# Kernel optimization log

Hardware: AMD Instinct MI355X
Metric: run time of the kernel (lower is better)

## Reference

```python
import jax, jax.numpy as jnp
import numpy as np


def _quantum_act(x, act_w):
    # LearnedQuantumActivation, eval mode (no phase noise): softmax-weighted mix of 9 activations
    w = jax.nn.softmax(act_w)
    mish = x * jnp.tanh(jax.nn.softplus(x))
    return (w[0] * jax.nn.sigmoid(x) + w[1] * jax.nn.elu(x) + w[2] * jnp.tanh(x)
            + w[3] * jax.nn.relu(x) + w[4] * jax.nn.silu(x)
            + w[5] * jax.nn.gelu(x, approximate=False) + w[6] * jax.nn.selu(x)
            + w[7] * mish + w[8] * x)


def setup_inputs() -> dict:
    B, D, U, N = 1024, 1024, 2048, 4      # batch, input_dim, max_units, num_branches
    M, MD, O, H = 2048, 1024, 512, 64     # memory_size, memory_dim, output_dim, critic hidden
    key = jax.random.key(0)
    ks = jax.random.split(key, 16)
    g = lambda k, shape, s=0.02: jax.random.normal(k, shape, dtype=jnp.float32) * s
    return {
        "x": jax.random.normal(ks[0], (B, D), dtype=jnp.float32),
        "w": g(ks[1], (D, U, N)),
        "b": jnp.zeros((U, N), jnp.float32),
        "gate_w": g(ks[2], (D, N)), "gate_b": jnp.zeros((N,), jnp.float32),
        "act_w": jnp.ones((9,), jnp.float32),
        "mask": jnp.ones((U,), jnp.float32),          # neuron_mask, initial_units == max_units
        "mem": g(ks[3], (M, MD), 0.05),
        "att_w": g(ks[4], (U, M)), "att_b": jnp.zeros((M,), jnp.float32),
        "write_w": g(ks[5], (U, MD)), "write_b": jnp.zeros((MD,), jnp.float32),
        "update_gate": jnp.full((M,), 0.5, jnp.float32),
        "out_w": g(ks[6], (U, O)), "out_b": jnp.zeros((O,), jnp.float32),
        "cw1": g(ks[7], (MD, H // 2)), "cb1": jnp.zeros((H // 2,), jnp.float32),
        "cw2": g(ks[8], (O, H // 2)), "cb2": jnp.zeros((H // 2,), jnp.float32),
        "cw3": g(ks[9], (U, H // 2)), "cb3": jnp.zeros((H // 2,), jnp.float32),
        "cw4": g(ks[10], (3 * (H // 2), H)), "cb4": jnp.zeros((H,), jnp.float32),
        "cw5": g(ks[11], (H, 2)), "cb5": jnp.zeros((2,), jnp.float32),
        "meta_threshold": jnp.float32(0.5),
    }


def reference(x, w, b, gate_w, gate_b, act_w, mask, mem, att_w, att_b,
              write_w, write_b, update_gate, out_w, out_b,
              cw1, cb1, cw2, cb2, cw3, cb3, cw4, cb4, cw5, cb5, meta_threshold):
    # Dendritic plastic dense: per-branch projections mixed by a learned softmax branch gate
    pre = jnp.einsum('bi,iun->bun', x, w) + b               # (B, U, N)
    gate = jax.nn.softmax(x @ gate_w + gate_b, axis=-1)     # (B, N)
    hidden = _quantum_act(jnp.einsum('bun,bn->bu', pre, gate), act_w) * mask  # (B, U)
    # Episodic memory read + write (write is returned instead of in-place assign)
    read_att = jax.nn.softmax(hidden @ att_w + att_b, axis=-1)  # (B, M)
    read = read_att @ mem                                       # (B, MD)
    cand = jnp.tanh(hidden @ write_w + write_b)                 # (B, MD)
    u = (jnp.mean(read_att, axis=0) * update_gate)[:, None]     # (M, 1)
    new_mem = mem * (1.0 - u) + u * jnp.mean(cand, axis=0)      # (M, MD)
    # Prediction head
    preds = hidden @ out_w + out_b                              # (B, O)
    # Metacognitive critic gating
    mf = jax.nn.relu(read @ cw1 + cb1)
    pf = jax.nn.relu(preds @ cw2 + cb2)
    hf = jax.nn.relu(hidden @ cw3 + cb3)
    fused = jax.nn.relu(jnp.concatenate([mf, pf, hf], axis=-1) @ cw4 + cb4)
    outs = fused @ cw5 + cb5
    gating = jax.nn.sigmoid(outs[:, 0:1] - meta_threshold)
    return (preds * gating, new_mem)
```

## Files before the change

### kernel.cpp

```cpp
#include <hip/hip_runtime.h>
#include <hip/hip_bf16.h>
#include <math.h>

typedef __attribute__((ext_vector_type(4))) float f32x4;
typedef __attribute__((ext_vector_type(8))) short s16x8;
typedef __attribute__((ext_vector_type(4))) short s16x4;
typedef __hip_bfloat16 bf16;

#define MB (1024ull*1024ull)
#define GATE_OFF    (0ull)
#define ACTW_OFF    (16ull*1024)
#define U_OFF       (20ull*1024)
#define CMEAN_OFF   (28ull*1024)
#define PART_OFF    (64ull*1024)
#define HIDDEN_OFF  (1ull*MB)
#define RATT_OFF    (5ull*MB)
#define CAND_OFF    (9ull*MB)
#define PREDS_OFF   (11ull*MB)
#define READ_OFF    (13ull*MB)
#define XBF_OFF     (17ull*MB)
#define WT_OFF      (19ull*MB)
#define CATT_OFF    (35ull*MB)
#define MEMT_OFF    (49ull*MB)
#define READ2_OFF   WT_OFF

__device__ __forceinline__ short f2bf_s(float f) {
    bf16 h = __float2bfloat16(f);
    return *reinterpret_cast<short*>(&h);
}

__device__ __forceinline__ void async_load16(const bf16* g, short* l) {
    __builtin_amdgcn_global_load_lds((const __attribute__((address_space(1))) void*)g,
                                     (__attribute__((address_space(3))) void*)l, 16, 0, 0);
}

__device__ __forceinline__ float fast_tanh(float x) {
    float e2x = __expf(2.f * x);
    return 1.f - 2.f / (e2x + 1.f);
}

__device__ __forceinline__ float qact(float x, const float* w) {
    float ex  = __expf(x);
    float r1  = 1.f / (1.f + ex);
    float sig = 1.f - r1;
    float em1 = ex - 1.f;
    float elu = x > 0.f ? x : em1;
    float e2x = ex * ex;
    float th  = 1.f - 2.f / (e2x + 1.f);
    float rel = fmaxf(x, 0.f);
    float silu = x * sig;
    float u   = 0.7978845608028654f * (x + 0.044715f * x * x * x);
    float e2u = __expf(2.f * u);
    float gel = x * (1.f - 1.f / (e2u + 1.f));
    float sel = 1.0507009873554805f * (x > 0.f ? x : 1.6732632423543772f * em1);
    float t   = 1.f + ex;
    float t2  = t * t;
    float mish = x * (1.f - 2.f / (t2 + 1.f));
    return w[0]*sig + w[1]*elu + w[2]*th + w[3]*rel + w[4]*silu
         + w[5]*gel + w[6]*sel + w[7]*mish + w[8]*x;
}

__device__ __forceinline__ void do_transpose(const float* __restrict__ in,
                                             bf16* __restrict__ out, int R, int C,
                                             int bx, int by, int t, short* tile) {
    int k0 = by*64, n0 = bx*64;
    int tx = t & 63, ty = t >> 6;
    #pragma unroll
    for (int j = 0; j < 16; j++) {
        int k = ty + j*4;
        tile[tx*66 + k] = f2bf_s(in[(size_t)(k0 + k)*C + n0 + tx]);
    }
    __syncthreads();
    int kp = t & 31, nrow = t >> 5;
    #pragma unroll
    for (int jj = 0; jj < 8; jj++) {
        int n = nrow + jj*8;
        unsigned lo = (unsigned short)tile[n*66 + kp*2];
        unsigned hi = (unsigned short)tile[n*66 + kp*2 + 1];
        *reinterpret_cast<unsigned*>(&out[(size_t)(n0 + n)*R + k0 + kp*2]) = lo | (hi << 16);
    }
}

__global__ __launch_bounds__(256) void k_prepass(
        const float* __restrict__ x, bf16* __restrict__ xbf,
        const float* __restrict__ gw, const float* __restrict__ gb,
        const float* __restrict__ aw_in,
        float* __restrict__ gate, float* __restrict__ actw,
        const float* __restrict__ w_, bf16* __restrict__ wT) {
    __shared__ short tile[64*66];
    int blk = blockIdx.x, t = threadIdx.x;
    if (blk < 1024) {
        int i = blk*256 + t;
        f32x4 v = ((const f32x4*)x)[i];
        s16x4 o;
        #pragma unroll
        for (int j = 0; j < 4; j++) o[j] = f2bf_s(v[j]);
        ((s16x4*)xbf)[i] = o;
        if (blk == 0 && t == 64) {
            float a[9]; float m = -1e30f;
            for (int i2 = 0; i2 < 9; i2++) { a[i2] = aw_in[i2]; m = fmaxf(m, a[i2]); }
            float ss = 0.f;
            for (int i2 = 0; i2 < 9; i2++) { a[i2] = __expf(a[i2]-m); ss += a[i2]; }
            float inv = 1.f / ss;
            for (int i2 = 0; i2 < 9; i2++) actw[i2] = a[i2]*inv;
        }
    } else if (blk < 2048) {
        int b = blk - 1024, w = t >> 6, lane = t & 63;
        __shared__ float l[4];
        float s = 0.f;
        for (int k = lane; k < 1024; k += 64)
            s += x[(size_t)b*1024 + k] * gw[k*4 + w];
        #pragma unroll
        for (int off = 32; off; off >>= 1) s += __shfl_xor(s, off);
        if (lane == 0) l[w] = s + gb[w];
        __syncthreads();
        if (t == 0) {
            float m = fmaxf(fmaxf(l[0], l[1]), fmaxf(l[2], l[3]));
            float e0 = __expf(l[0]-m), e1 = __expf(l[1]-m), e2 = __expf(l[2]-m), e3 = __expf(l[3]-m);
            float inv = 1.f / (e0+e1+e2+e3);
            gate[b*4+0] = e0*inv; gate[b*4+1] = e1*inv;
            gate[b*4+2] = e2*inv; gate[b*4+3] = e3*inv;
        }
    } else {
        int rel = blk - 2048;
        do_transpose(w_, wT, 1024, 8192, rel & 127, rel >> 7, t, tile);
    }
}

template <int TM>
union SMemT {
    struct { short a[2][TM*32]; short b[2][128*32]; } tl;
    float z[TM*32];
    short tr[64*66];
};

template <int MODE, int TM>
__device__ __forceinline__ void gemm_core(
        int bx, int by, int bz, SMemT<TM>& sm,
        const bf16* __restrict__ A, const bf16* __restrict__ Bt,
        int K, int lda, int ldb, int kOffset,
        const float* __restrict__ bias, const float* __restrict__ bias2,
        const float* __restrict__ bias3,
        float* __restrict__ outF, float* __restrict__ outF2,
        bf16* __restrict__ outH, bf16* __restrict__ outH2,
        const float* __restrict__ gate, const float* __restrict__ actw,
        const float* __restrict__ mask, int outStride) {
    constexpr int MI = TM / 32;
    int t = threadIdx.x, lane = t & 63;
    int rowBase = by * TM, colBase = bx * 128;
    int lm = lane & 15, lq = lane >> 4;
    int w = t >> 6;
    int qm = (w >> 1) * (TM/2), qn = (w & 1) * 64;

    A  += (size_t)kOffset * bz;
    Bt += (size_t)kOffset * bz;

    f32x4 acc[MI][4];
    #pragma unroll
    for (int i = 0; i < MI; i++)
        #pragma unroll
        for (int j = 0; j < 4; j++) acc[i][j] = (f32x4){0.f, 0.f, 0.f, 0.f};

    int cb0 = w*128 + lane, cb1 = cb0 + 64;
    int rb0 = cb0 >> 2, kb0 = (cb0 & 3) * 8;
    int rb1 = cb1 >> 2, kb1 = (cb1 & 3) * 8;
    int ca0 = (TM == 128) ? (w*128 + lane) : (w*64 + lane);
    int ra0 = ca0 >> 2, ka0 = (ca0 & 3) * 8;
    int ra1 = (ca0 + 64) >> 2, ka1 = ((ca0 + 64) & 3) * 8;

    auto issueLoads = [&](int k0, int ib) {
        short* bA = sm.tl.a[ib];
        short* bB = sm.tl.b[ib];
        async_load16(A + (size_t)(rowBase + ra0)*lda + k0 + ka0,
                     bA + ((TM == 128) ? w*1024 : w*512));
        if (TM == 128)
            async_load16(A + (size_t)(rowBase + ra1)*lda + k0 + ka1, bA + w*1024 + 512);
        async_load16(Bt + (size_t)(colBase + rb0)*ldb + k0 + kb0, bB + w*1024);
        async_load16(Bt + (size_t)(colBase + rb1)*ldb + k0 + kb1, bB + w*1024 + 512);
    };

    issueLoads(0, 0);
    int ib = 0;
    for (int k0 = 0; k0 < K; k0 += 32) {
        __syncthreads();
        if (k0 + 32 < K) issueLoads(k0 + 32, ib ^ 1);
        const short* cA = sm.tl.a[ib];
        const short* cB = sm.tl.b[ib];
        s16x8 af[MI], bfr[4];
        #pragma unroll
        for (int mi = 0; mi < MI; mi++)
            af[mi] = *reinterpret_cast<const s16x8*>(cA + (qm + mi*16 + lm)*32 + lq*8);
        #pragma unroll
        for (int ni = 0; ni < 4; ni++)
            bfr[ni] = *reinterpret_cast<const s16x8*>(cB + (qn + ni*16 + lm)*32 + lq*8);
        #pragma unroll
        for (int mi = 0; mi < MI; mi++)
            #pragma unroll
            for (int ni = 0; ni < 4; ni++)
                acc[mi][ni] = __builtin_amdgcn_mfma_f32_16x16x32_bf16(af[mi], bfr[ni], acc[mi][ni], 0, 0, 0);
        ib ^= 1;
    }

    if (MODE == 4) {
        __syncthreads();
        #pragma unroll
        for (int mi = 0; mi < MI; mi++) {
            int rowl0 = qm + mi*16 + lq*4;
            #pragma unroll
            for (int ni = 0; ni < 4; ni++) {
                int col = colBase + qn + ni*16 + lm;
                int n = col & 3;
                float bb = bias[col];
                f32x4 v = acc[mi][ni];
                #pragma unroll
                for (int r = 0; r < 4; r++) v[r] = (v[r] + bb) * gate[(rowBase + rowl0 + r)*4 + n];
                #pragma unroll
                for (int r = 0; r < 4; r++) v[r] += __shfl_xor(v[r], 1);
                #pragma unroll
                for (int r = 0; r < 4; r++) v[r] += __shfl_xor(v[r], 2);
                if ((lane & 3) == 0) {
                    int ul = ((w & 1) << 4) + ni*4 + (lm >> 2);
                    #pragma unroll
                    for (int r = 0; r < 4; r++)
                        sm.z[(rowl0 + r)*32 + ul] = v[r];
                }
            }
        }
        __syncthreads();
        float aw[9];
        #pragma unroll
        for (int i = 0; i < 9; i++) aw[i] = actw[i];
        int u0 = colBase >> 2;
        #pragma unroll
        for (int i = 0; i < TM/8; i++) {
            int idx = t + i*256;
            int row = idx >> 5, ul = idx & 31;
            int ug = u0 + ul;
            float zz = sm.z[idx];
            outH[(size_t)(rowBase + row)*outStride + ug] = __float2bfloat16(qact(zz, aw) * mask[ug]);
        }
    } else if (MODE == 5) {
        #pragma unroll
        for (int mi = 0; mi < MI; mi++) {
            int row0 = rowBase + qm + mi*16 + lq*4;
            #pragma unroll
            for (int ni = 0; ni < 4; ni++) {
                int col = colBase + qn + ni*16 + lm;
                if (col < 2048) {
                    float bb = bias[col];
                    #pragma unroll
                    for (int r = 0; r < 4; r++)
                        outH[(size_t)(row0 + r)*2048 + col] = __float2bfloat16(acc[mi][ni][r] + bb);
                } else if (col < 3072) {
                    int c = col - 2048;
                    float bb = bias2[c];
                    #pragma unroll
                    for (int r = 0; r < 4; r++)
                        outH2[(size_t)(row0 + r)*1024 + c] = __float2bfloat16(fast_tanh(acc[mi][ni][r] + bb));
                } else {
                    int c = col - 3072;
                    float bb = bias3[c];
                    #pragma unroll
                    for (int r = 0; r < 4; r++)
                        outF[(size_t)(row0 + r)*512 + c] = acc[mi][ni][r] + bb;
                }
            }
        }
    } else {
        float* of = bz ? (outF2 + (size_t)(bz - 1) * 1048576) : outF;
        #pragma unroll
        for (int mi = 0; mi < MI; mi++) {
            int row0 = rowBase + qm + mi*16 + lq*4;
            #pragma unroll
            for (int ni = 0; ni < 4; ni++) {
                int col = colBase + qn + ni*16 + lm;
                #pragma unroll
                for (int r = 0; r < 4; r++)
                    of[(size_t)(row0 + r)*outStride + col] = acc[mi][ni][r];
            }
        }
    }
}

template <int MODE, int TM>
__global__ __launch_bounds__(256, 2) void gemm_bt(
        const bf16* __restrict__ A, const bf16* __restrict__ Bt,
        int K, int lda, int ldb, int kOffset,
        const float* __restrict__ bias, const float* __restrict__ bias2,
        const float* __restrict__ bias3,
        float* __restrict__ outF, float* __restrict__ outF2,
        bf16* __restrict__ outH, bf16* __restrict__ outH2,
        const float* __restrict__ gate, const float* __restrict__ actw,
        const float* __restrict__ mask, int outStride) {
    __shared__ __align__(16) SMemT<TM> sm;
    gemm_core<MODE, TM>(blockIdx.x, blockIdx.y, blockIdx.z, sm,
                        A, Bt, K, lda, ldb, kOffset, bias, bias2, bias3,
                        outF, outF2, outH, outH2, gate, actw, mask, outStride);
}

__global__ __launch_bounds__(256, 2) void k_g1x(
        const bf16* __restrict__ xbf, const bf16* __restrict__ wT,
        const float* __restrict__ bias, bf16* __restrict__ hidden,
        const float* __restrict__ gate, const float* __restrict__ actw,
        const float* __restrict__ mask,
        const float* __restrict__ att_w, const float* __restrict__ write_w,
        const float* __restrict__ out_w, bf16* __restrict__ catT,
        const float* __restrict__ mem, bf16* __restrict__ memT) {
    __shared__ __align__(16) SMemT<128> sm;
    int bid = blockIdx.x, t = threadIdx.x;
    if (bid < 512) {
        gemm_core<4, 128>(bid & 63, bid >> 6, 0, sm, xbf, wT, 1024, 1024, 1024, 0,
                          bias, nullptr, nullptr, nullptr, nullptr, hidden, nullptr,
                          gate, actw, mask, 2048);
    } else {
        int rel = bid - 512;
        if (rel < 1024) {
            do_transpose(att_w, catT, 2048, 2048, rel & 31, rel >> 5, t, sm.tr);
        } else if (rel < 1536) {
            rel -= 1024;
            do_transpose(write_w, catT + 2048ull*2048, 2048, 1024, rel & 15, rel >> 4, t, sm.tr);
        } else if (rel < 1792) {
            rel -= 1536;
            do_transpose(out_w, catT + 3072ull*2048, 2048, 512, rel & 7, rel >> 3, t, sm.tr);
        } else {
            rel -= 1792;
            do_transpose(mem, memT, 2048, 1024, rel & 15, rel >> 4, t, sm.tr);
        }
    }
}

__global__ __launch_bounds__(256) void k_softmax(bf16* __restrict__ ratt) {
    int b = blockIdx.x, t = threadIdx.x, w = t >> 6, lane = t & 63;
    __shared__ float red[8];
    bf16* row = ratt + (size_t)b*2048;
    float v[8];
    float mx = -1e30f;
    #pragma unroll
    for (int j = 0; j < 8; j++) {
        v[j] = __bfloat162float(row[t + j*256]);
        mx = fmaxf(mx, v[j]);
    }
    #pragma unroll
    for (int off = 32; off; off >>= 1) mx = fmaxf(mx, __shfl_xor(mx, off));
    if (lane == 0) red[w] = mx;
    __syncthreads();
    mx = fmaxf(fmaxf(red[0], red[1]), fmaxf(red[2], red[3]));
    float s = 0.f;
    #pragma unroll
    for (int j = 0; j < 8; j++) { v[j] = __expf(v[j] - mx); s += v[j]; }
    #pragma unroll
    for (int off = 32; off; off >>= 1) s += __shfl_xor(s, off);
    if (lane == 0) red[4 + w] = s;
    __syncthreads();
    float inv = 1.f / (red[4] + red[5] + red[6] + red[7]);
    #pragma unroll
    for (int j = 0; j < 8; j++)
        row[t + j*256] = __float2bfloat16(v[j] * inv);
}

__global__ __launch_bounds__(256) void k_colpart(const bf16* __restrict__ ratt,
                                                 const bf16* __restrict__ cand,
                                                 float* __restrict__ part) {
    int ct = blockIdx.x, rc = blockIdx.y, t = threadIdx.x;
    int col = ct*256 + t;
    const bf16* src; int stride, c;
    if (ct < 8) { src = ratt; stride = 2048; c = col; }
    else        { src = cand; stride = 1024; c = col - 2048; }
    float s = 0.f;
    int r0 = rc*128;
    for (int r = 0; r < 128; r++)
        s += __bfloat162float(src[(size_t)(r0 + r)*stride + c]);
    part[rc*3072 + col] = s;
}

__global__ __launch_bounds__(256) void k_colfin(const float* __restrict__ part,
                                                const float* __restrict__ update_gate,
                                                float* __restrict__ u,
                                                float* __restrict__ cmean) {
    int col = blockIdx.x*256 + threadIdx.x;
    float s = 0.f;
    #pragma unroll
    for (int rc = 0; rc < 8; rc++) s += part[rc*3072 + col];
    s *= (1.f/1024.f);
    if (col < 2048) u[col] = s * update_gate[col];
    else            cmean[col - 2048] = s;
}

__global__ __launch_bounds__(256) void k_newmem(const float* __restrict__ mem,
                                                const float* __restrict__ u,
                                                const float* __restrict__ cmean,
                                                float* __restrict__ out1) {
    int idx = blockIdx.x*256 + threadIdx.x;
    int m = idx >> 10, d = idx & 1023;
    float um = u[m];
    out1[idx] = mem[idx] * (1.f - um) + um * cmean[d];
}

__global__ __launch_bounds__(256) void k_critic(
        const float* __restrict__ readv, const float* __restrict__ readv2,
        const float* __restrict__ preds, const bf16* __restrict__ hidden,
        const float* cw1, const float* cb1, const float* cw2, const float* cb2,
        const float* cw3, const float* cb3, const float* cw4, const float* cb4,
        const float* cw5, const float* cb5, const float* thr,
        float* __restrict__ out0) {
    __shared__ __align__(16) float sx[2*1024];
    __shared__ __align__(16) float sp[2*512];
    __shared__ __align__(16) short sh[2*2048];
    __shared__ __align__(16) f32x4 part[2][32][8];
    __shared__ float feat[2][96];
    __shared__ float fused[2][64];
    __shared__ float gsh[2];
    int b0 = blockIdx.x * 2, t = threadIdx.x;
    int j4 = t & 7, kg = t >> 3;

    {
        const f32x4* r0 = (const f32x4*)(readv  + (size_t)b0*1024);
        const f32x4* r1 = (const f32x4*)(readv2 + (size_t)b0*1024);
        const f32x4* r2 = (const f32x4*)(readv2 + 1048576 + (size_t)b0*1024);
        const f32x4* r3 = (const f32x4*)(readv2 + 2097152 + (size_t)b0*1024);
        ((f32x4*)sx)[t]       = r0[t] + r1[t] + r2[t] + r3[t];
        ((f32x4*)sx)[t + 256] = r0[t + 256] + r1[t + 256] + r2[t + 256] + r3[t + 256];
    }
    ((f32x4*)sp)[t]       = ((const f32x4*)(preds + (size_t)b0*512))[t];
    ((s16x8*)sh)[t]       = ((const s16x8*)(hidden + (size_t)b0*2048))[t];
    ((s16x8*)sh)[t + 256] = ((const s16x8*)(hidden + (size_t)b0*2048))[t + 256];
    __syncthreads();

    {
        const f32x4* wv = (const f32x4*)cw1;
        f32x4 a0 = (f32x4){0,0,0,0}, a1 = (f32x4){0,0,0,0};
        int k0 = kg*32;
        #pragma unroll 4
        for (int k = k0; k < k0 + 32; k++) {
            f32x4 wq = wv[k*8 + j4];
            a0 += sx[k] * wq;
            a1 += sx[1024 + k] * wq;
        }
        part[0][kg][j4] = a0; part[1][kg][j4] = a1;
    }
    __syncthreads();
    if (t < 64) {
        int r = t >> 5, f = t & 31;
        float s = 0.f;
        #pragma unroll
        for (int i = 0; i < 32; i++) s += part[r][i][f >> 2][f & 3];
        feat[r][f] = fmaxf(s + cb1[f], 0.f);
    }
    __syncthreads();
    {
        const f32x4* wv = (const f32x4*)cw2;
        f32x4 a0 = (f32x4){0,0,0,0}, a1 = (f32x4){0,0,0,0};
        int k0 = kg*16;
        #pragma unroll 4
        for (int k = k0; k < k0 + 16; k++) {
            f32x4 wq = wv[k*8 + j4];
            a0 += sp[k] * wq;
            a1 += sp[512 + k] * wq;
        }
        part[0][kg][j4] = a0; part[1][kg][j4] = a1;
    }
    __syncthreads();
    if (t < 64) {
        int r = t >> 5, f = t & 31;
        float s = 0.f;
        #pragma unroll
        for (int i = 0; i < 32; i++) s += part[r][i][f >> 2][f & 3];
        feat[r][32 + f] = fmaxf(s + cb2[f], 0.f);
    }
    __syncthreads();
    {
        const f32x4* wv = (const f32x4*)cw3;
        f32x4 a0 = (f32x4){0,0,0,0}, a1 = (f32x4){0,0,0,0};
        int k0 = kg*64;
        #pragma unroll 4
        for (int k = k0; k < k0 + 64; k++) {
            f32x4 wq = wv[k*8 + j4];
            float h0 = __bfloat162float(*reinterpret_cast<const bf16*>(&sh[k]));
            float h1 = __bfloat162float(*reinterpret_cast<const bf16*>(&sh[2048 + k]));
            a0 += h0 * wq;
            a1 += h1 * wq;
        }
        part[0][kg][j4] = a0; part[1][kg][j4] = a1;
    }
    __syncthreads();
    if (t < 64) {
        int r = t >> 5, f = t & 31;
        float s = 0.f;
        #pragma unroll
        for (int i = 0; i < 32; i++) s += part[r][i][f >> 2][f & 3];
        feat[r][64 + f] = fmaxf(s + cb3[f], 0.f);
    }
    __syncthreads();
    if (t < 128) {
        int r = t >> 6, uu = t & 63;
        float s = 0.f;
        #pragma unroll 8
        for (int k = 0; k < 96; k++) s += feat[r][k] * cw4[k*64 + uu];
        fused[r][uu] = fmaxf(s + cb4[uu], 0.f);
    }
    __syncthreads();
    if (t < 128) {
        int r = t >> 6, lane = t & 63;
        float v = fused[r][lane] * cw5[lane*2];
        #pragma unroll
        for (int off = 32; off; off >>= 1) v += __shfl_xor(v, off);
        if (lane == 0)
            gsh[r] = 1.f / (1.f + __expf(-(v + cb5[0] - thr[0])));
    }
    __syncthreads();
    #pragma unroll
    for (int idx = t; idx < 1024; idx += 256) {
        int r = idx >> 9, o = idx & 511;
        out0[(size_t)(b0 + r)*512 + o] = sp[r*512 + o] * gsh[r];
    }
}

extern "C" void kernel_launch(void* const* d_in, const int* in_sizes, int n_in,
                              void* d_out, int out_size, void* d_ws, size_t ws_size,
                              hipStream_t stream) {
    const float* x        = (const float*)d_in[0];
    const float* w_       = (const float*)d_in[1];
    const float* b_bias   = (const float*)d_in[2];
    const float* gate_w   = (const float*)d_in[3];
    const float* gate_b   = (const float*)d_in[4];
    const float* act_w    = (const float*)d_in[5];
    const float* mask     = (const float*)d_in[6];
    const float* mem      = (const float*)d_in[7];
    const float* att_w    = (const float*)d_in[8];
    const float* att_b    = (const float*)d_in[9];
    const float* write_w  = (const float*)d_in[10];
    const float* write_b  = (const float*)d_in[11];
    const float* upd_gate = (const float*)d_in[12];
    const float* out_w    = (const float*)d_in[13];
    const float* out_b    = (const float*)d_in[14];
    const float* cw1 = (const float*)d_in[15]; const float* cb1 = (const float*)d_in[16];
    const float* cw2 = (const float*)d_in[17]; const float* cb2 = (const float*)d_in[18];
    const float* cw3 = (const float*)d_in[19]; const float* cb3 = (const float*)d_in[20];
    const float* cw4 = (const float*)d_in[21]; const float* cb4 = (const float*)d_in[22];
    const float* cw5 = (const float*)d_in[23]; const float* cb5 = (const float*)d_in[24];
    const float* thr = (const float*)d_in[25];

    char* ws = (char*)d_ws;
    float* gate   = (float*)(ws + GATE_OFF);
    float* actw   = (float*)(ws + ACTW_OFF);
    float* uvec   = (float*)(ws + U_OFF);
    float* cmean  = (float*)(ws + CMEAN_OFF);
    float* part   = (float*)(ws + PART_OFF);
    bf16*  hidden = (bf16*)(ws + HIDDEN_OFF);
    bf16*  ratt   = (bf16*)(ws + RATT_OFF);
    bf16*  cand   = (bf16*)(ws + CAND_OFF);
    float* preds  = (float*)(ws + PREDS_OFF);
    float* readv  = (float*)(ws + READ_OFF);
    float* readv2 = (float*)(ws + READ2_OFF);
    bf16*  xbf    = (bf16*)(ws + XBF_OFF);
    bf16*  wT     = (bf16*)(ws + WT_OFF);
    bf16*  catT   = (bf16*)(ws + CATT_OFF);
    bf16*  memT   = (bf16*)(ws + MEMT_OFF);

    float* out0 = (float*)d_out;
    float* out1 = out0 + 1024*512;

    k_prepass<<<4096, 256, 0, stream>>>(x, xbf, gate_w, gate_b, act_w, gate, actw, w_, wT);

    k_g1x<<<2816, 256, 0, stream>>>(xbf, wT, b_bias, hidden, gate, actw, mask,
                                    att_w, write_w, out_w, catT, mem, memT);

    gemm_bt<5, 64><<<dim3(28, 16), 256, 0, stream>>>(hidden, catT, 2048, 2048, 2048, 0,
        att_b, write_b, out_b, preds, nullptr, ratt, cand, nullptr, nullptr, nullptr, 0);
    k_softmax<<<1024, 256, 0, stream>>>(ratt);
    gemm_bt<3, 64><<<dim3(8, 16, 4), 256, 0, stream>>>(ratt, memT, 512, 2048, 2048, 512,
        nullptr, nullptr, nullptr, readv, readv2, nullptr, nullptr, nullptr, nullptr, nullptr, 1024);

    k_colpart<<<dim3(12, 8), 256, 0, stream>>>(ratt, cand, part);
    k_colfin<<<12, 256, 0, stream>>>(part, upd_gate, uvec, cmean);
    k_newmem<<<8192, 256, 0, stream>>>(mem, uvec, cmean, out1);
    k_critic<<<512, 256, 0, stream>>>(readv, readv2, preds, hidden,
        cw1, cb1, cw2, cb2, cw3, cb3, cw4, cb4, cw5, cb5, thr, out0);
}
```

Baseline: 269.7 us.

## Co-schedule independent kernels into shared launches and interleave GEMM with transposes

The first fused kernel now interleaves its GEMM blocks with the weight/mem transpose blocks (2 of every 11) so that compute-bound and memory-bound work run side by side instead of in separate phases. The read GEMM and the column-partial reductions are merged into one launch. The new_mem update, now vectorised to float4, is merged with the critic into a single launch. This removes two kernel launches and their tail gaps, and lets independent work overlap. The cost is more branching and heterogeneous blocks that share the larger kernel's LDS and register footprint.

```diff
diff --git a/kernel.cpp b/kernel.cpp
--- a/kernel.cpp
+++ b/kernel.cpp
@@ -308,12 +308,14 @@
         const float* __restrict__ mem, bf16* __restrict__ memT) {
     __shared__ __align__(16) SMemT<128> sm;
     int bid = blockIdx.x, t = threadIdx.x;
-    if (bid < 512) {
-        gemm_core<4, 128>(bid & 63, bid >> 6, 0, sm, xbf, wT, 1024, 1024, 1024, 0,
+    int g = bid / 11, r = bid % 11;
+    if (r < 2) {
+        int gid = g*2 + r;
+        gemm_core<4, 128>(gid & 63, gid >> 6, 0, sm, xbf, wT, 1024, 1024, 1024, 0,
                           bias, nullptr, nullptr, nullptr, nullptr, hidden, nullptr,
                           gate, actw, mask, 2048);
     } else {
-        int rel = bid - 512;
+        int rel = g*9 + (r - 2);
         if (rel < 1024) {
             do_transpose(att_w, catT, 2048, 2048, rel & 31, rel >> 5, t, sm.tr);
         } else if (rel < 1536) {
@@ -358,19 +360,31 @@
         row[t + j*256] = __float2bfloat16(v[j] * inv);
 }
 
-__global__ __launch_bounds__(256) void k_colpart(const bf16* __restrict__ ratt,
-                                                 const bf16* __restrict__ cand,
-                                                 float* __restrict__ part) {
-    int ct = blockIdx.x, rc = blockIdx.y, t = threadIdx.x;
-    int col = ct*256 + t;
-    const bf16* src; int stride, c;
-    if (ct < 8) { src = ratt; stride = 2048; c = col; }
-    else        { src = cand; stride = 1024; c = col - 2048; }
-    float s = 0.f;
-    int r0 = rc*128;
-    for (int r = 0; r < 128; r++)
-        s += __bfloat162float(src[(size_t)(r0 + r)*stride + c]);
-    part[rc*3072 + col] = s;
+__global__ __launch_bounds__(256, 2) void k_g5x(
+        const bf16* __restrict__ ratt, const bf16* __restrict__ memT,
+        const bf16* __restrict__ cand,
+        float* __restrict__ readv, float* __restrict__ readv2,
+        float* __restrict__ part) {
+    __shared__ __align__(16) SMemT<64> sm;
+    int bid = blockIdx.x, t = threadIdx.x;
+    if (bid < 512) {
+        int bx = bid & 7, by = (bid >> 3) & 15, bz = bid >> 7;
+        gemm_core<3, 64>(bx, by, bz, sm, ratt, memT, 512, 2048, 2048, 512,
+                         nullptr, nullptr, nullptr, readv, readv2, nullptr, nullptr,
+                         nullptr, nullptr, nullptr, 1024);
+    } else {
+        int rel = bid - 512;
+        int ct = rel % 12, rc = rel / 12;
+        int col = ct*256 + t;
+        const bf16* src; int stride, c;
+        if (ct < 8) { src = ratt; stride = 2048; c = col; }
+        else        { src = cand; stride = 1024; c = col - 2048; }
+        float s = 0.f;
+        int r0 = rc*128;
+        for (int r2 = 0; r2 < 128; r2++)
+            s += __bfloat162float(src[(size_t)(r0 + r2)*stride + c]);
+        part[rc*3072 + col] = s;
+    }
 }
 
 __global__ __launch_bounds__(256) void k_colfin(const float* __restrict__ part,
@@ -386,23 +400,15 @@
     else            cmean[col - 2048] = s;
 }
 
-__global__ __launch_bounds__(256) void k_newmem(const float* __restrict__ mem,
-                                                const float* __restrict__ u,
-                                                const float* __restrict__ cmean,
-                                                float* __restrict__ out1) {
-    int idx = blockIdx.x*256 + threadIdx.x;
-    int m = idx >> 10, d = idx & 1023;
-    float um = u[m];
-    out1[idx] = mem[idx] * (1.f - um) + um * cmean[d];
-}
-
-__global__ __launch_bounds__(256) void k_critic(
+__global__ __launch_bounds__(256) void k_fin(
         const float* __restrict__ readv, const float* __restrict__ readv2,
         const float* __restrict__ preds, const bf16* __restrict__ hidden,
         const float* cw1, const float* cb1, const float* cw2, const float* cb2,
         const float* cw3, const float* cb3, const float* cw4, const float* cb4,
         const float* cw5, const float* cb5, const float* thr,
-        float* __restrict__ out0) {
+        float* __restrict__ out0,
+        const float* __restrict__ mem, const float* __restrict__ u,
+        const float* __restrict__ cmean, float* __restrict__ out1) {
     __shared__ __align__(16) float sx[2*1024];
     __shared__ __align__(16) float sp[2*512];
     __shared__ __align__(16) short sh[2*2048];
@@ -410,7 +416,20 @@
     __shared__ float feat[2][96];
     __shared__ float fused[2][64];
     __shared__ float gsh[2];
-    int b0 = blockIdx.x * 2, t = threadIdx.x;
+    int bid = blockIdx.x, t = threadIdx.x;
+    if (bid >= 512) {
+        int idx = (bid - 512)*256 + t;
+        int m = idx >> 8, d4 = idx & 255;
+        float um = u[m];
+        f32x4 m4 = ((const f32x4*)mem)[idx];
+        f32x4 c4 = ((const f32x4*)cmean)[d4];
+        f32x4 o;
+        #pragma unroll
+        for (int j = 0; j < 4; j++) o[j] = m4[j] * (1.f - um) + um * c4[j];
+        ((f32x4*)out1)[idx] = o;
+        return;
+    }
+    int b0 = bid * 2;
     int j4 = t & 7, kg = t >> 3;
 
     {
@@ -568,12 +587,10 @@
     gemm_bt<5, 64><<<dim3(28, 16), 256, 0, stream>>>(hidden, catT, 2048, 2048, 2048, 0,
         att_b, write_b, out_b, preds, nullptr, ratt, cand, nullptr, nullptr, nullptr, 0);
     k_softmax<<<1024, 256, 0, stream>>>(ratt);
-    gemm_bt<3, 64><<<dim3(8, 16, 4), 256, 0, stream>>>(ratt, memT, 512, 2048, 2048, 512,
-        nullptr, nullptr, nullptr, readv, readv2, nullptr, nullptr, nullptr, nullptr, nullptr, 1024);
-
-    k_colpart<<<dim3(12, 8), 256, 0, stream>>>(ratt, cand, part);
+    k_g5x<<<608, 256, 0, stream>>>(ratt, memT, cand, readv, readv2, part);
+
     k_colfin<<<12, 256, 0, stream>>>(part, upd_gate, uvec, cmean);
-    k_newmem<<<8192, 256, 0, stream>>>(mem, uvec, cmean, out1);
-    k_critic<<<512, 256, 0, stream>>>(readv, readv2, preds, hidden,
-        cw1, cb1, cw2, cb2, cw3, cb3, cw4, cb4, cw5, cb5, thr, out0);
-}
+    k_fin<<<2560, 256, 0, stream>>>(readv, readv2, preds, hidden,
+        cw1, cb1, cw2, cb2, cw3, cb3, cw4, cb4, cw5, cb5, thr, out0,
+        mem, uvec, cmean, out1);
+}
```

New measurement: 269.3 us. Within noise of the previous version (-0.2%).
